# Kernel tuning notes

Measured on AMD Instinct MI355X. Metric: run time of the kernel, lower is better.

The kernel has to match this reference:

```python
import jax, jax.numpy as jnp
import numpy as np

N = 100000
E = 800000
IN_FEATS = 128
H_FEATS = 128
HEADS = 4
OUT = H_FEATS // HEADS  # 32
NEG_SLOPE = 0.2  # DGL GATConv default


def gat_conv(x, src, dst, W, attn_l, attn_r, bias):
    """DGL-style GATConv. x: [N, F_in] -> [N, HEADS, OUT]."""
    h = (x @ W).reshape(N, HEADS, OUT)                      # projected features
    el = jnp.sum(h * attn_l, axis=-1)                       # [N, H]
    er = jnp.sum(h * attn_r, axis=-1)                       # [N, H]
    e = jax.nn.leaky_relu(el[src] + er[dst], NEG_SLOPE)     # [E, H] edge logits
    # edge softmax over incoming edges of each dst node
    m = jax.ops.segment_max(e, dst, num_segments=N)          # [N, H]
    ex = jnp.exp(e - m[dst])                                 # [E, H]
    s = jax.ops.segment_sum(ex, dst, num_segments=N)         # [N, H]
    a = ex / s[dst]                                          # [E, H]
    msg = h[src] * a[:, :, None]                             # [E, H, OUT]
    out = jax.ops.segment_sum(msg, dst, num_segments=N)      # [N, H, OUT]
    return out + bias.reshape(1, HEADS, OUT)


def setup_inputs() -> dict:
    key = jax.random.key(0)
    ks = jax.random.split(key, 12)
    feat = jax.random.normal(ks[0], (N, IN_FEATS), dtype=jnp.float32)
    src = jax.random.randint(ks[1], (E,), 0, N)
    dst = jax.random.randint(ks[2], (E,), 0, N)
    s1 = 1.0 / np.sqrt(IN_FEATS)
    s2 = 1.0 / np.sqrt(H_FEATS)
    return {
        "feat": feat,
        "src": src,
        "dst": dst,
        "W1": jax.random.normal(ks[3], (IN_FEATS, HEADS * OUT), dtype=jnp.float32) * s1,
        "al1": jax.random.normal(ks[4], (HEADS, OUT), dtype=jnp.float32) * s2,
        "ar1": jax.random.normal(ks[5], (HEADS, OUT), dtype=jnp.float32) * s2,
        "b1": jnp.zeros((HEADS * OUT,), dtype=jnp.float32),
        "W2": jax.random.normal(ks[6], (H_FEATS, HEADS * OUT), dtype=jnp.float32) * s2,
        "al2": jax.random.normal(ks[7], (HEADS, OUT), dtype=jnp.float32) * s2,
        "ar2": jax.random.normal(ks[8], (HEADS, OUT), dtype=jnp.float32) * s2,
        "b2": jnp.zeros((HEADS * OUT,), dtype=jnp.float32),
    }


def reference(feat, src, dst, W1, al1, ar1, b1, W2, al2, ar2, b2):
    h = gat_conv(feat, src, dst, W1, al1, ar1, b1).reshape(N, H_FEATS)  # flatten(1)
    h = jax.nn.relu(h)
    h = gat_conv(h, src, dst, W2, al2, ar2, b2).mean(axis=1)            # mean over heads
    return h
```

## Files before the change

kernel.cpp:

```cpp
#include <hip/hip_runtime.h>
#include <math.h>

#define N_NODES 100000
#define N_EDGES 800000
#define NEG_SLOPE 0.2f

typedef __attribute__((ext_vector_type(8))) short short8;
typedef __attribute__((ext_vector_type(4))) float floatx4;

__device__ __forceinline__ float lrelu(float x) { return x > 0.f ? x : NEG_SLOPE * x; }

__device__ __forceinline__ unsigned bf16_rne(float f) {
    unsigned u = __float_as_uint(f);
    return (u + 0x7fffu + ((u >> 16) & 1u)) >> 16;
}
__device__ __forceinline__ unsigned bfpack(float lo, float hi) {
    return bf16_rne(lo) | (bf16_rne(hi) << 16);
}
__device__ __forceinline__ float bflo(unsigned p) { return __uint_as_float(p << 16); }
__device__ __forceinline__ float bfhi(unsigned p) { return __uint_as_float(p & 0xffff0000u); }

__global__ void k_hist(const int* __restrict__ dst, int* __restrict__ deg) {
    int e = blockIdx.x * blockDim.x + threadIdx.x;
    if (e < N_EDGES) atomicAdd(&deg[dst[e]], 1);
}

__global__ __launch_bounds__(256) void k_scan1(const int* __restrict__ deg,
                                               int* __restrict__ rs,
                                               int* __restrict__ bsums) {
    __shared__ int sd[256];
    int tid = threadIdx.x;
    int base = blockIdx.x * 1024 + tid * 4;
    int v0 = (base + 0 < N_NODES) ? deg[base + 0] : 0;
    int v1 = (base + 1 < N_NODES) ? deg[base + 1] : 0;
    int v2 = (base + 2 < N_NODES) ? deg[base + 2] : 0;
    int v3 = (base + 3 < N_NODES) ? deg[base + 3] : 0;
    int t = v0 + v1 + v2 + v3;
    sd[tid] = t;
    __syncthreads();
    int incl = t;
    for (int off = 1; off < 256; off <<= 1) {
        int x = (tid >= off) ? sd[tid - off] : 0;
        __syncthreads();
        incl += x;
        sd[tid] = incl;
        __syncthreads();
    }
    int excl = incl - t;
    if (base + 0 < N_NODES) rs[base + 0] = excl;
    if (base + 1 < N_NODES) rs[base + 1] = excl + v0;
    if (base + 2 < N_NODES) rs[base + 2] = excl + v0 + v1;
    if (base + 3 < N_NODES) rs[base + 3] = excl + v0 + v1 + v2;
    if (tid == 255) bsums[blockIdx.x] = incl;
}

__global__ __launch_bounds__(256) void k_scan2(int* __restrict__ bs, int nb) {
    __shared__ int sd[256];
    int tid = threadIdx.x;
    int t = (tid < nb) ? bs[tid] : 0;
    sd[tid] = t;
    __syncthreads();
    int incl = t;
    for (int off = 1; off < 256; off <<= 1) {
        int x = (tid >= off) ? sd[tid - off] : 0;
        __syncthreads();
        incl += x;
        sd[tid] = incl;
        __syncthreads();
    }
    if (tid < nb) bs[tid] = incl - t;
}

__global__ void k_scan3(int* __restrict__ rs, const int* __restrict__ bs,
                        int* __restrict__ cursor) {
    int idx = blockIdx.x * blockDim.x + threadIdx.x;
    if (idx < N_NODES) {
        int v = rs[idx] + bs[idx >> 10];
        rs[idx] = v;
        cursor[idx] = v;
    }
    if (idx == 0) rs[N_NODES] = N_EDGES;
}

__global__ void k_scatter(const int* __restrict__ src, const int* __restrict__ dst,
                          int* __restrict__ cursor, int* __restrict__ csr_src) {
    int e = blockIdx.x * blockDim.x + threadIdx.x;
    if (e < N_EDGES) {
        int d = dst[e];
        int p = atomicAdd(&cursor[d], 1);
        csr_src[p] = src[e];
    }
}

__global__ __launch_bounds__(256) void k_wprep2(const float* __restrict__ W1,
                                                const float* __restrict__ W2,
                                                unsigned short* __restrict__ wt1,
                                                unsigned short* __restrict__ wt2) {
    int tid = blockIdx.x * 256 + threadIdx.x;
    const float* W = (tid < 16384) ? W1 : W2;
    unsigned short* wt = (tid < 16384) ? wt1 : wt2;
    int t = tid & 16383;
    int n = t >> 7, k = t & 127;
    wt[t] = (unsigned short)bf16_rne(W[k * 128 + n]);
}

__global__ __launch_bounds__(256) void k_gemm(const void* __restrict__ Xv,
                                              const unsigned short* __restrict__ wt,
                                              const float* __restrict__ al,
                                              const float* __restrict__ ar,
                                              unsigned* __restrict__ Hb,
                                              float* __restrict__ EL,
                                              float* __restrict__ ER,
                                              int src_bf16) {
    __shared__ unsigned short wsh[128 * 128];
    int tid = threadIdx.x;
    int w = tid >> 6, lane = tid & 63;
    int q = lane >> 4, nl = lane & 15;
    int base = blockIdx.x * 128;

    const uint4* wt4 = (const uint4*)wt;
    #pragma unroll
    for (int i = 0; i < 8; i++) {
        int idx = tid + i * 256;
        int rn = idx >> 4, c8 = idx & 15;
        int kc = c8 >> 2, qq = c8 & 3;
        int slot = rn * 128 + ((kc ^ ((rn >> 2) & 3)) * 4 + (qq ^ (rn & 3))) * 8;
        *(uint4*)&wsh[slot] = wt4[idx];
    }

    short8 afr[2][4];
    int row0 = base + w * 32 + nl;
    if (!src_bf16) {
        const float4* X4 = (const float4*)Xv;
        #pragma unroll
        for (int rt = 0; rt < 2; rt++) {
            int rr = row0 + rt * 16; if (rr > N_NODES - 1) rr = N_NODES - 1;
            const float4* px = X4 + (size_t)rr * 32 + q * 2;
            #pragma unroll
            for (int kc = 0; kc < 4; kc++) {
                float4 u = px[kc * 8], v = px[kc * 8 + 1];
                short8 f;
                f[0] = (short)bf16_rne(u.x); f[1] = (short)bf16_rne(u.y);
                f[2] = (short)bf16_rne(u.z); f[3] = (short)bf16_rne(u.w);
                f[4] = (short)bf16_rne(v.x); f[5] = (short)bf16_rne(v.y);
                f[6] = (short)bf16_rne(v.z); f[7] = (short)bf16_rne(v.w);
                afr[rt][kc] = f;
            }
        }
    } else {
        const unsigned short* Xb = (const unsigned short*)Xv;
        #pragma unroll
        for (int rt = 0; rt < 2; rt++) {
            int rr = row0 + rt * 16; if (rr > N_NODES - 1) rr = N_NODES - 1;
            #pragma unroll
            for (int kc = 0; kc < 4; kc++)
                afr[rt][kc] = *(const short8*)(Xb + (size_t)rr * 128 + kc * 32 + q * 8);
        }
    }

    floatx4 acc[2][8];
    #pragma unroll
    for (int rt = 0; rt < 2; rt++)
        #pragma unroll
        for (int ct = 0; ct < 8; ct++)
            acc[rt][ct] = (floatx4){0.f, 0.f, 0.f, 0.f};

    __syncthreads();

    int sw_hi = (nl >> 2) & 3, sw_lo = nl & 3;
    #pragma unroll
    for (int ct = 0; ct < 8; ct++) {
        int rbase = (ct * 16 + nl) * 128;
        #pragma unroll
        for (int kc = 0; kc < 4; kc++) {
            short8 b = *(const short8*)&wsh[rbase + ((kc ^ sw_hi) * 4 + (q ^ sw_lo)) * 8];
            acc[0][ct] = __builtin_amdgcn_mfma_f32_16x16x32_bf16(afr[0][kc], b, acc[0][ct], 0, 0, 0);
            acc[1][ct] = __builtin_amdgcn_mfma_f32_16x16x32_bf16(afr[1][kc], b, acc[1][ct], 0, 0, 0);
        }
    }

    float all_[4], alh_[4], arl_[4], arh_[4];
    #pragma unroll
    for (int h = 0; h < 4; h++) {
        all_[h] = al[h * 32 + nl]; alh_[h] = al[h * 32 + 16 + nl];
        arl_[h] = ar[h * 32 + nl]; arh_[h] = ar[h * 32 + 16 + nl];
    }
    #pragma unroll
    for (int rt = 0; rt < 2; rt++) {
        #pragma unroll
        for (int r = 0; r < 4; r++) {
            int row = base + w * 32 + rt * 16 + q * 4 + r;
            bool valid = row < N_NODES;
            unsigned* hrow = Hb + (size_t)row * 64;
            #pragma unroll
            for (int ct = 0; ct < 8; ct++) {
                float vlo = acc[rt][ct][r];
                float vhi = __shfl_down(vlo, 1);
                if (valid && !(nl & 1)) hrow[ct * 8 + (nl >> 1)] = bfpack(vlo, vhi);
            }
            #pragma unroll
            for (int h = 0; h < 4; h++) {
                float pel = acc[rt][2 * h][r] * all_[h] + acc[rt][2 * h + 1][r] * alh_[h];
                float per = acc[rt][2 * h][r] * arl_[h] + acc[rt][2 * h + 1][r] * arh_[h];
                #pragma unroll
                for (int o = 1; o < 16; o <<= 1) {
                    pel += __shfl_xor(pel, o);
                    per += __shfl_xor(per, o);
                }
                if (valid && nl == 0) { EL[row * 4 + h] = pel; ER[row * 4 + h] = per; }
            }
        }
    }
}

__global__ __launch_bounds__(256) void k_gather(const int* __restrict__ rs,
                                                const int* __restrict__ csr_src,
                                                const float* __restrict__ EL,
                                                const float* __restrict__ ER,
                                                const unsigned* __restrict__ Hb,
                                                const float* __restrict__ bias,
                                                void* __restrict__ out,
                                                int final_layer) {
    int wid = (blockIdx.x * blockDim.x + threadIdx.x) >> 6;
    int lane = threadIdx.x & 63;
    int g = lane >> 4, l16 = lane & 15;
    int h = l16 >> 2;
    int n0 = wid * 4;
    if (n0 >= N_NODES) return;
    int nend = min(n0 + 4, N_NODES);

    float bv[8];
    #pragma unroll
    for (int c = 0; c < 8; c++) bv[c] = bias[l16 * 8 + c];

    for (int n = n0; n < nend; n++) {
        int s = rs[n], e = rs[n + 1];
        float erh = ER[n * 4 + h];
        float acc[8];
        #pragma unroll
        for (int c = 0; c < 8; c++) acc[c] = 0.f;
        float sa = 0.f;

        for (int j = s; j < e; j += 8) {
            int j0 = j + g, j1 = j + 4 + g;
            uint4 p0 = make_uint4(0, 0, 0, 0), p1 = make_uint4(0, 0, 0, 0);
            float w0 = 0.f, w1 = 0.f;
            if (j0 < e) {
                int s0 = csr_src[j0];
                p0 = *(const uint4*)(Hb + (size_t)s0 * 64 + l16 * 4);
                w0 = __expf(lrelu(EL[s0 * 4 + h] + erh));
            }
            if (j1 < e) {
                int s1 = csr_src[j1];
                p1 = *(const uint4*)(Hb + (size_t)s1 * 64 + l16 * 4);
                w1 = __expf(lrelu(EL[s1 * 4 + h] + erh));
            }
            sa += w0 + w1;
            acc[0] = fmaf(bflo(p0.x), w0, acc[0]); acc[1] = fmaf(bfhi(p0.x), w0, acc[1]);
            acc[2] = fmaf(bflo(p0.y), w0, acc[2]); acc[3] = fmaf(bfhi(p0.y), w0, acc[3]);
            acc[4] = fmaf(bflo(p0.z), w0, acc[4]); acc[5] = fmaf(bfhi(p0.z), w0, acc[5]);
            acc[6] = fmaf(bflo(p0.w), w0, acc[6]); acc[7] = fmaf(bfhi(p0.w), w0, acc[7]);
            acc[0] = fmaf(bflo(p1.x), w1, acc[0]); acc[1] = fmaf(bfhi(p1.x), w1, acc[1]);
            acc[2] = fmaf(bflo(p1.y), w1, acc[2]); acc[3] = fmaf(bfhi(p1.y), w1, acc[3]);
            acc[4] = fmaf(bflo(p1.z), w1, acc[4]); acc[5] = fmaf(bfhi(p1.z), w1, acc[5]);
            acc[6] = fmaf(bflo(p1.w), w1, acc[6]); acc[7] = fmaf(bfhi(p1.w), w1, acc[7]);
        }

        #pragma unroll
        for (int c = 0; c < 8; c++) {
            acc[c] += __shfl_xor(acc[c], 16);
            acc[c] += __shfl_xor(acc[c], 32);
        }
        sa += __shfl_xor(sa, 16);
        sa += __shfl_xor(sa, 32);
        float inv = (e > s) ? 1.f / sa : 0.f;

        float r[8];
        #pragma unroll
        for (int c = 0; c < 8; c++) r[c] = acc[c] * inv + bv[c];

        if (!final_layer) {
            if (g == 0) {
                uint4 pk;
                pk.x = bfpack(fmaxf(r[0], 0.f), fmaxf(r[1], 0.f));
                pk.y = bfpack(fmaxf(r[2], 0.f), fmaxf(r[3], 0.f));
                pk.z = bfpack(fmaxf(r[4], 0.f), fmaxf(r[5], 0.f));
                pk.w = bfpack(fmaxf(r[6], 0.f), fmaxf(r[7], 0.f));
                *(uint4*)((unsigned*)out + (size_t)n * 64 + l16 * 4) = pk;
            }
        } else {
            #pragma unroll
            for (int c = 0; c < 8; c++) {
                r[c] += __shfl_xor(r[c], 4);
                r[c] += __shfl_xor(r[c], 8);
            }
            if (g == 0 && l16 < 4) {
                float* po = (float*)out + (size_t)n * 32 + l16 * 8;
                *(float4*)po = make_float4(0.25f * r[0], 0.25f * r[1], 0.25f * r[2], 0.25f * r[3]);
                *(float4*)(po + 4) = make_float4(0.25f * r[4], 0.25f * r[5], 0.25f * r[6], 0.25f * r[7]);
            }
        }
    }
}

extern "C" void kernel_launch(void* const* d_in, const int* in_sizes, int n_in,
                              void* d_out, int out_size, void* d_ws, size_t ws_size,
                              hipStream_t stream) {
    const float* feat = (const float*)d_in[0];
    const int* src = (const int*)d_in[1];
    const int* dst = (const int*)d_in[2];
    const float* W1 = (const float*)d_in[3];
    const float* al1 = (const float*)d_in[4];
    const float* ar1 = (const float*)d_in[5];
    const float* b1 = (const float*)d_in[6];
    const float* W2 = (const float*)d_in[7];
    const float* al2 = (const float*)d_in[8];
    const float* ar2 = (const float*)d_in[9];
    const float* b2 = (const float*)d_in[10];
    float* out = (float*)d_out;

    char* ws = (char*)d_ws;
    size_t off = 0;
    auto alloc = [&](size_t bytes) {
        void* p = ws + off;
        off += (bytes + 255) & ~(size_t)255;
        return p;
    };
    int* deg = (int*)alloc((size_t)N_NODES * 4);
    int* rs = (int*)alloc(((size_t)N_NODES + 1) * 4);
    int* cursor = (int*)alloc((size_t)N_NODES * 4);
    int* bsums = (int*)alloc(128 * 4);
    int* csr_src = (int*)alloc((size_t)N_EDGES * 4);
    unsigned* Hb = (unsigned*)alloc((size_t)N_NODES * 64 * 4);
    float* el = (float*)alloc((size_t)N_NODES * 4 * 4);
    float* er = (float*)alloc((size_t)N_NODES * 4 * 4);
    unsigned* out1b = (unsigned*)alloc((size_t)N_NODES * 64 * 4);
    unsigned short* wt1 = (unsigned short*)alloc(128 * 128 * 2);
    unsigned short* wt2 = (unsigned short*)alloc(128 * 128 * 2);

    hipMemsetAsync(deg, 0, (size_t)N_NODES * 4, stream);

    k_hist<<<(N_EDGES + 255) / 256, 256, 0, stream>>>(dst, deg);
    k_scan1<<<98, 256, 0, stream>>>(deg, rs, bsums);
    k_scan2<<<1, 256, 0, stream>>>(bsums, 98);
    k_scan3<<<(N_NODES + 255) / 256, 256, 0, stream>>>(rs, bsums, cursor);
    k_scatter<<<(N_EDGES + 255) / 256, 256, 0, stream>>>(src, dst, cursor, csr_src);
    k_wprep2<<<128, 256, 0, stream>>>(W1, W2, wt1, wt2);

    int gemm_blocks = (N_NODES + 127) / 128;
    int gat_blocks = (N_NODES + 15) / 16;

    k_gemm<<<gemm_blocks, 256, 0, stream>>>(feat, wt1, al1, ar1, Hb, el, er, 0);
    k_gather<<<gat_blocks, 256, 0, stream>>>(rs, csr_src, el, er, Hb, b1, out1b, 0);
    k_gemm<<<gemm_blocks, 256, 0, stream>>>(out1b, wt2, al2, ar2, Hb, el, er, 1);
    k_gather<<<gat_blocks, 256, 0, stream>>>(rs, csr_src, el, er, Hb, b2, out, 1);
}
```

Before: 338.6 us.

## Fuse preprocessing kernels, single-pass decoupled scan, and prefetch next node's first edges in gather

Merges the degree histogram and weight bf16 conversion into one launch. It replaces the three-kernel scan with one kernel that publishes block sums and spin-waits on a global counter, which relies on all 98 blocks being resident at once. In the gather kernel, the first batch of each next node's edges (csr index, feature row, EL) is loaded early to overlap latency with the current node's work. Together these cut launch count and serial latency, at the cost of a grid-wide spin barrier and higher register use.

```diff
diff --git a/kernel.cpp b/kernel.cpp
--- a/kernel.cpp
+++ b/kernel.cpp
@@ -20,17 +20,44 @@
 __device__ __forceinline__ float bflo(unsigned p) { return __uint_as_float(p << 16); }
 __device__ __forceinline__ float bfhi(unsigned p) { return __uint_as_float(p & 0xffff0000u); }
 
-__global__ void k_hist(const int* __restrict__ dst, int* __restrict__ deg) {
-    int e = blockIdx.x * blockDim.x + threadIdx.x;
-    if (e < N_EDGES) atomicAdd(&deg[dst[e]], 1);
-}
-
-__global__ __launch_bounds__(256) void k_scan1(const int* __restrict__ deg,
-                                               int* __restrict__ rs,
-                                               int* __restrict__ bsums) {
+#define ACC8(P, W)                                                   \
+    acc[0] = fmaf(bflo((P).x), (W), acc[0]);                         \
+    acc[1] = fmaf(bfhi((P).x), (W), acc[1]);                         \
+    acc[2] = fmaf(bflo((P).y), (W), acc[2]);                         \
+    acc[3] = fmaf(bfhi((P).y), (W), acc[3]);                         \
+    acc[4] = fmaf(bflo((P).z), (W), acc[4]);                         \
+    acc[5] = fmaf(bfhi((P).z), (W), acc[5]);                         \
+    acc[6] = fmaf(bflo((P).w), (W), acc[6]);                         \
+    acc[7] = fmaf(bfhi((P).w), (W), acc[7]);
+
+__global__ __launch_bounds__(256) void k_hist_wprep(const int* __restrict__ dst,
+                                                    int* __restrict__ deg,
+                                                    const float* __restrict__ W1,
+                                                    const float* __restrict__ W2,
+                                                    unsigned short* __restrict__ wt1,
+                                                    unsigned short* __restrict__ wt2) {
+    int b = blockIdx.x;
+    if (b < 3125) {
+        int e = b * 256 + threadIdx.x;
+        if (e < N_EDGES) atomicAdd(&deg[dst[e]], 1);
+    } else {
+        int tid = (b - 3125) * 256 + threadIdx.x;
+        const float* W = (tid < 16384) ? W1 : W2;
+        unsigned short* wt = (tid < 16384) ? wt1 : wt2;
+        int t = tid & 16383;
+        int n = t >> 7, k = t & 127;
+        wt[t] = (unsigned short)bf16_rne(W[k * 128 + n]);
+    }
+}
+
+__global__ __launch_bounds__(256) void k_scan(const int* __restrict__ deg,
+                                              int* __restrict__ rs,
+                                              int* __restrict__ cursor,
+                                              int* __restrict__ bsums,
+                                              int* __restrict__ done) {
     __shared__ int sd[256];
-    int tid = threadIdx.x;
-    int base = blockIdx.x * 1024 + tid * 4;
+    int tid = threadIdx.x, b = blockIdx.x;
+    int base = b * 1024 + tid * 4;
     int v0 = (base + 0 < N_NODES) ? deg[base + 0] : 0;
     int v1 = (base + 1 < N_NODES) ? deg[base + 1] : 0;
     int v2 = (base + 2 < N_NODES) ? deg[base + 2] : 0;
@@ -47,39 +74,33 @@
         __syncthreads();
     }
     int excl = incl - t;
-    if (base + 0 < N_NODES) rs[base + 0] = excl;
-    if (base + 1 < N_NODES) rs[base + 1] = excl + v0;
-    if (base + 2 < N_NODES) rs[base + 2] = excl + v0 + v1;
-    if (base + 3 < N_NODES) rs[base + 3] = excl + v0 + v1 + v2;
-    if (tid == 255) bsums[blockIdx.x] = incl;
-}
-
-__global__ __launch_bounds__(256) void k_scan2(int* __restrict__ bs, int nb) {
-    __shared__ int sd[256];
-    int tid = threadIdx.x;
-    int t = (tid < nb) ? bs[tid] : 0;
-    sd[tid] = t;
-    __syncthreads();
-    int incl = t;
-    for (int off = 1; off < 256; off <<= 1) {
-        int x = (tid >= off) ? sd[tid - off] : 0;
+
+    if (tid == 255) {
+        atomicExch(&bsums[b], incl);
+        __threadfence();
+        atomicAdd(done, 1);
+    }
+    if (tid == 0) {
+        while (atomicAdd(done, 0) < 98) { }
+    }
+    __syncthreads();
+
+    int bv = (tid < b) ? atomicAdd(&bsums[tid], 0) : 0;
+    __syncthreads();
+    sd[tid] = bv;
+    __syncthreads();
+    for (int off = 128; off > 0; off >>= 1) {
+        if (tid < off) sd[tid] += sd[tid + off];
         __syncthreads();
-        incl += x;
-        sd[tid] = incl;
-        __syncthreads();
-    }
-    if (tid < nb) bs[tid] = incl - t;
-}
-
-__global__ void k_scan3(int* __restrict__ rs, const int* __restrict__ bs,
-                        int* __restrict__ cursor) {
-    int idx = blockIdx.x * blockDim.x + threadIdx.x;
-    if (idx < N_NODES) {
-        int v = rs[idx] + bs[idx >> 10];
-        rs[idx] = v;
-        cursor[idx] = v;
-    }
-    if (idx == 0) rs[N_NODES] = N_EDGES;
+    }
+    int boff = sd[0];
+
+    int p0 = excl + boff;
+    if (base + 0 < N_NODES) { rs[base + 0] = p0; cursor[base + 0] = p0; }
+    if (base + 1 < N_NODES) { rs[base + 1] = p0 + v0; cursor[base + 1] = p0 + v0; }
+    if (base + 2 < N_NODES) { rs[base + 2] = p0 + v0 + v1; cursor[base + 2] = p0 + v0 + v1; }
+    if (base + 3 < N_NODES) { rs[base + 3] = p0 + v0 + v1 + v2; cursor[base + 3] = p0 + v0 + v1 + v2; }
+    if (b == 0 && tid == 0) rs[N_NODES] = N_EDGES;
 }
 
 __global__ void k_scatter(const int* __restrict__ src, const int* __restrict__ dst,
@@ -90,18 +111,6 @@
         int p = atomicAdd(&cursor[d], 1);
         csr_src[p] = src[e];
     }
-}
-
-__global__ __launch_bounds__(256) void k_wprep2(const float* __restrict__ W1,
-                                                const float* __restrict__ W2,
-                                                unsigned short* __restrict__ wt1,
-                                                unsigned short* __restrict__ wt2) {
-    int tid = blockIdx.x * 256 + threadIdx.x;
-    const float* W = (tid < 16384) ? W1 : W2;
-    unsigned short* wt = (tid < 16384) ? wt1 : wt2;
-    int t = tid & 16383;
-    int n = t >> 7, k = t & 127;
-    wt[t] = (unsigned short)bf16_rne(W[k * 128 + n]);
 }
 
 __global__ __launch_bounds__(256) void k_gemm(const void* __restrict__ Xv,
@@ -214,7 +223,7 @@
 }
 
 __global__ __launch_bounds__(256) void k_gather(const int* __restrict__ rs,
-                                                const int* __restrict__ csr_src,
+                                                const int* __restrict__ csr,
                                                 const float* __restrict__ EL,
                                                 const float* __restrict__ ER,
                                                 const unsigned* __restrict__ Hb,
@@ -227,43 +236,73 @@
     int h = l16 >> 2;
     int n0 = wid * 4;
     if (n0 >= N_NODES) return;
-    int nend = min(n0 + 4, N_NODES);
+    int nlast = min(4, N_NODES - n0);
 
     float bv[8];
     #pragma unroll
     for (int c = 0; c < 8; c++) bv[c] = bias[l16 * 8 + c];
 
-    for (int n = n0; n < nend; n++) {
-        int s = rs[n], e = rs[n + 1];
-        float erh = ER[n * 4 + h];
-        float acc[8];
-        #pragma unroll
-        for (int c = 0; c < 8; c++) acc[c] = 0.f;
-        float sa = 0.f;
-
-        for (int j = s; j < e; j += 8) {
+    int sE[5];
+    #pragma unroll
+    for (int i = 0; i < 5; i++) sE[i] = rs[min(n0 + i, N_NODES)];
+    float erh[4];
+    #pragma unroll
+    for (int i = 0; i < 4; i++) erh[i] = (n0 + i < N_NODES) ? ER[(n0 + i) * 4 + h] : 0.f;
+
+    const uint4 zero4 = make_uint4(0, 0, 0, 0);
+
+    int cs0 = 0, cs1 = 0; bool cv0, cv1;
+    {
+        int s = sE[0], e = sE[1];
+        cv0 = (s + g) < e; cv1 = (s + 4 + g) < e;
+        if (cv0) cs0 = csr[s + g];
+        if (cv1) cs1 = csr[s + 4 + g];
+    }
+    uint4 cp0 = zero4, cp1 = zero4;
+    float cel0 = 0.f, cel1 = 0.f;
+    if (cv0) { cp0 = *(const uint4*)(Hb + (size_t)cs0 * 64 + l16 * 4); cel0 = EL[cs0 * 4 + h]; }
+    if (cv1) { cp1 = *(const uint4*)(Hb + (size_t)cs1 * 64 + l16 * 4); cel1 = EL[cs1 * 4 + h]; }
+
+    for (int nn = 0; nn < nlast; nn++) {
+        int s = sE[nn], e = sE[nn + 1];
+
+        int ns0 = 0, ns1 = 0; bool nv0 = false, nv1 = false;
+        if (nn + 1 < nlast) {
+            int s2 = sE[nn + 1], e2 = sE[nn + 2];
+            nv0 = (s2 + g) < e2; nv1 = (s2 + 4 + g) < e2;
+            if (nv0) ns0 = csr[s2 + g];
+            if (nv1) ns1 = csr[s2 + 4 + g];
+        }
+
+        float acc[8] = {0.f, 0.f, 0.f, 0.f, 0.f, 0.f, 0.f, 0.f};
+        float w0 = cv0 ? __expf(lrelu(cel0 + erh[nn])) : 0.f;
+        float w1 = cv1 ? __expf(lrelu(cel1 + erh[nn])) : 0.f;
+        float sa = w0 + w1;
+        ACC8(cp0, w0);
+        ACC8(cp1, w1);
+
+        for (int j = s + 8; j < e; j += 8) {
             int j0 = j + g, j1 = j + 4 + g;
-            uint4 p0 = make_uint4(0, 0, 0, 0), p1 = make_uint4(0, 0, 0, 0);
-            float w0 = 0.f, w1 = 0.f;
-            if (j0 < e) {
-                int s0 = csr_src[j0];
-                p0 = *(const uint4*)(Hb + (size_t)s0 * 64 + l16 * 4);
-                w0 = __expf(lrelu(EL[s0 * 4 + h] + erh));
-            }
-            if (j1 < e) {
-                int s1 = csr_src[j1];
-                p1 = *(const uint4*)(Hb + (size_t)s1 * 64 + l16 * 4);
-                w1 = __expf(lrelu(EL[s1 * 4 + h] + erh));
-            }
-            sa += w0 + w1;
-            acc[0] = fmaf(bflo(p0.x), w0, acc[0]); acc[1] = fmaf(bfhi(p0.x), w0, acc[1]);
-            acc[2] = fmaf(bflo(p0.y), w0, acc[2]); acc[3] = fmaf(bfhi(p0.y), w0, acc[3]);
-            acc[4] = fmaf(bflo(p0.z), w0, acc[4]); acc[5] = fmaf(bfhi(p0.z), w0, acc[5]);
-            acc[6] = fmaf(bflo(p0.w), w0, acc[6]); acc[7] = fmaf(bfhi(p0.w), w0, acc[7]);
-            acc[0] = fmaf(bflo(p1.x), w1, acc[0]); acc[1] = fmaf(bfhi(p1.x), w1, acc[1]);
-            acc[2] = fmaf(bflo(p1.y), w1, acc[2]); acc[3] = fmaf(bfhi(p1.y), w1, acc[3]);
-            acc[4] = fmaf(bflo(p1.z), w1, acc[4]); acc[5] = fmaf(bfhi(p1.z), w1, acc[5]);
-            acc[6] = fmaf(bflo(p1.w), w1, acc[6]); acc[7] = fmaf(bfhi(p1.w), w1, acc[7]);
+            bool b0 = j0 < e, b1 = j1 < e;
+            int t0 = 0, t1 = 0;
+            if (b0) t0 = csr[j0];
+            if (b1) t1 = csr[j1];
+            uint4 p0 = zero4, p1 = zero4;
+            float e0 = 0.f, e1 = 0.f;
+            if (b0) { p0 = *(const uint4*)(Hb + (size_t)t0 * 64 + l16 * 4); e0 = EL[t0 * 4 + h]; }
+            if (b1) { p1 = *(const uint4*)(Hb + (size_t)t1 * 64 + l16 * 4); e1 = EL[t1 * 4 + h]; }
+            float x0 = b0 ? __expf(lrelu(e0 + erh[nn])) : 0.f;
+            float x1 = b1 ? __expf(lrelu(e1 + erh[nn])) : 0.f;
+            sa += x0 + x1;
+            ACC8(p0, x0);
+            ACC8(p1, x1);
+        }
+
+        if (nn + 1 < nlast) {
+            cp0 = zero4; cp1 = zero4; cel0 = 0.f; cel1 = 0.f;
+            if (nv0) { cp0 = *(const uint4*)(Hb + (size_t)ns0 * 64 + l16 * 4); cel0 = EL[ns0 * 4 + h]; }
+            if (nv1) { cp1 = *(const uint4*)(Hb + (size_t)ns1 * 64 + l16 * 4); cel1 = EL[ns1 * 4 + h]; }
+            cv0 = nv0; cv1 = nv1;
         }
 
         #pragma unroll
@@ -275,6 +314,7 @@
         sa += __shfl_xor(sa, 32);
         float inv = (e > s) ? 1.f / sa : 0.f;
 
+        int n = n0 + nn;
         float r[8];
         #pragma unroll
         for (int c = 0; c < 8; c++) r[c] = acc[c] * inv + bv[c];
@@ -327,6 +367,7 @@
         return p;
     };
     int* deg = (int*)alloc((size_t)N_NODES * 4);
+    int* done = (int*)alloc(256);
     int* rs = (int*)alloc(((size_t)N_NODES + 1) * 4);
     int* cursor = (int*)alloc((size_t)N_NODES * 4);
     int* bsums = (int*)alloc(128 * 4);
@@ -338,14 +379,12 @@
     unsigned short* wt1 = (unsigned short*)alloc(128 * 128 * 2);
     unsigned short* wt2 = (unsigned short*)alloc(128 * 128 * 2);
 
-    hipMemsetAsync(deg, 0, (size_t)N_NODES * 4, stream);
-
-    k_hist<<<(N_EDGES + 255) / 256, 256, 0, stream>>>(dst, deg);
-    k_scan1<<<98, 256, 0, stream>>>(deg, rs, bsums);
-    k_scan2<<<1, 256, 0, stream>>>(bsums, 98);
-    k_scan3<<<(N_NODES + 255) / 256, 256, 0, stream>>>(rs, bsums, cursor);
+    size_t zbytes = (size_t)((char*)done - (char*)deg) + 256;
+    hipMemsetAsync(deg, 0, zbytes, stream);
+
+    k_hist_wprep<<<3125 + 128, 256, 0, stream>>>(dst, deg, W1, W2, wt1, wt2);
+    k_scan<<<98, 256, 0, stream>>>(deg, rs, cursor, bsums, done);
     k_scatter<<<(N_EDGES + 255) / 256, 256, 0, stream>>>(src, dst, cursor, csr_src);
-    k_wprep2<<<128, 256, 0, stream>>>(W1, W2, wt1, wt2);
 
     int gemm_blocks = (N_NODES + 127) / 128;
     int gat_blocks = (N_NODES + 15) / 16;
```

After: 362.9 us. 7.2% more time.

## Merge preprocessing kernels and stage GEMM input tiles through shared memory

Applied to the files above, without the earlier changes.

Fuses the degree histogram with weight conversion into one launch, and replaces the three-kernel scan with a single kernel that uses a spin-wait grid barrier on an atomic counter to pick up the block offsets. This cuts kernel launches and the gaps between them. The GEMM now loads its input rows cooperatively with coalesced wide loads into a swizzled shared-memory tile before building MFMA fragments. That doubles shared memory use per block, which may lower occupancy, and the spin barrier assumes all 98 scan blocks are resident at once.

```diff
diff --git a/kernel.cpp b/kernel.cpp
--- a/kernel.cpp
+++ b/kernel.cpp
@@ -20,17 +20,34 @@
 __device__ __forceinline__ float bflo(unsigned p) { return __uint_as_float(p << 16); }
 __device__ __forceinline__ float bfhi(unsigned p) { return __uint_as_float(p & 0xffff0000u); }
 
-__global__ void k_hist(const int* __restrict__ dst, int* __restrict__ deg) {
-    int e = blockIdx.x * blockDim.x + threadIdx.x;
-    if (e < N_EDGES) atomicAdd(&deg[dst[e]], 1);
-}
-
-__global__ __launch_bounds__(256) void k_scan1(const int* __restrict__ deg,
-                                               int* __restrict__ rs,
-                                               int* __restrict__ bsums) {
+__global__ __launch_bounds__(256) void k_hist_wprep(const int* __restrict__ dst,
+                                                    int* __restrict__ deg,
+                                                    const float* __restrict__ W1,
+                                                    const float* __restrict__ W2,
+                                                    unsigned short* __restrict__ wt1,
+                                                    unsigned short* __restrict__ wt2) {
+    int b = blockIdx.x;
+    if (b < 3125) {
+        int e = b * 256 + threadIdx.x;
+        if (e < N_EDGES) atomicAdd(&deg[dst[e]], 1);
+    } else {
+        int tid = (b - 3125) * 256 + threadIdx.x;
+        const float* W = (tid < 16384) ? W1 : W2;
+        unsigned short* wt = (tid < 16384) ? wt1 : wt2;
+        int t = tid & 16383;
+        int n = t >> 7, k = t & 127;
+        wt[t] = (unsigned short)bf16_rne(W[k * 128 + n]);
+    }
+}
+
+__global__ __launch_bounds__(256) void k_scan(const int* __restrict__ deg,
+                                              int* __restrict__ rs,
+                                              int* __restrict__ cursor,
+                                              int* __restrict__ bsums,
+                                              int* __restrict__ done) {
     __shared__ int sd[256];
-    int tid = threadIdx.x;
-    int base = blockIdx.x * 1024 + tid * 4;
+    int tid = threadIdx.x, b = blockIdx.x;
+    int base = b * 1024 + tid * 4;
     int v0 = (base + 0 < N_NODES) ? deg[base + 0] : 0;
     int v1 = (base + 1 < N_NODES) ? deg[base + 1] : 0;
     int v2 = (base + 2 < N_NODES) ? deg[base + 2] : 0;
@@ -47,39 +64,33 @@
         __syncthreads();
     }
     int excl = incl - t;
-    if (base + 0 < N_NODES) rs[base + 0] = excl;
-    if (base + 1 < N_NODES) rs[base + 1] = excl + v0;
-    if (base + 2 < N_NODES) rs[base + 2] = excl + v0 + v1;
-    if (base + 3 < N_NODES) rs[base + 3] = excl + v0 + v1 + v2;
-    if (tid == 255) bsums[blockIdx.x] = incl;
-}
-
-__global__ __launch_bounds__(256) void k_scan2(int* __restrict__ bs, int nb) {
-    __shared__ int sd[256];
-    int tid = threadIdx.x;
-    int t = (tid < nb) ? bs[tid] : 0;
-    sd[tid] = t;
-    __syncthreads();
-    int incl = t;
-    for (int off = 1; off < 256; off <<= 1) {
-        int x = (tid >= off) ? sd[tid - off] : 0;
+
+    if (tid == 255) {
+        atomicExch(&bsums[b], incl);
+        __threadfence();
+        atomicAdd(done, 1);
+    }
+    if (tid == 0) {
+        while (atomicAdd(done, 0) < 98) { }
+    }
+    __syncthreads();
+
+    int bv = (tid < b) ? atomicAdd(&bsums[tid], 0) : 0;
+    __syncthreads();
+    sd[tid] = bv;
+    __syncthreads();
+    for (int off = 128; off > 0; off >>= 1) {
+        if (tid < off) sd[tid] += sd[tid + off];
         __syncthreads();
-        incl += x;
-        sd[tid] = incl;
-        __syncthreads();
-    }
-    if (tid < nb) bs[tid] = incl - t;
-}
-
-__global__ void k_scan3(int* __restrict__ rs, const int* __restrict__ bs,
-                        int* __restrict__ cursor) {
-    int idx = blockIdx.x * blockDim.x + threadIdx.x;
-    if (idx < N_NODES) {
-        int v = rs[idx] + bs[idx >> 10];
-        rs[idx] = v;
-        cursor[idx] = v;
-    }
-    if (idx == 0) rs[N_NODES] = N_EDGES;
+    }
+    int boff = sd[0];
+
+    int p0 = excl + boff;
+    if (base + 0 < N_NODES) { rs[base + 0] = p0; cursor[base + 0] = p0; }
+    if (base + 1 < N_NODES) { rs[base + 1] = p0 + v0; cursor[base + 1] = p0 + v0; }
+    if (base + 2 < N_NODES) { rs[base + 2] = p0 + v0 + v1; cursor[base + 2] = p0 + v0 + v1; }
+    if (base + 3 < N_NODES) { rs[base + 3] = p0 + v0 + v1 + v2; cursor[base + 3] = p0 + v0 + v1 + v2; }
+    if (b == 0 && tid == 0) rs[N_NODES] = N_EDGES;
 }
 
 __global__ void k_scatter(const int* __restrict__ src, const int* __restrict__ dst,
@@ -90,18 +101,6 @@
         int p = atomicAdd(&cursor[d], 1);
         csr_src[p] = src[e];
     }
-}
-
-__global__ __launch_bounds__(256) void k_wprep2(const float* __restrict__ W1,
-                                                const float* __restrict__ W2,
-                                                unsigned short* __restrict__ wt1,
-                                                unsigned short* __restrict__ wt2) {
-    int tid = blockIdx.x * 256 + threadIdx.x;
-    const float* W = (tid < 16384) ? W1 : W2;
-    unsigned short* wt = (tid < 16384) ? wt1 : wt2;
-    int t = tid & 16383;
-    int n = t >> 7, k = t & 127;
-    wt[t] = (unsigned short)bf16_rne(W[k * 128 + n]);
 }
 
 __global__ __launch_bounds__(256) void k_gemm(const void* __restrict__ Xv,
@@ -113,6 +112,7 @@
                                               float* __restrict__ ER,
                                               int src_bf16) {
     __shared__ unsigned short wsh[128 * 128];
+    __shared__ unsigned short xsh[128 * 128];
     int tid = threadIdx.x;
     int w = tid >> 6, lane = tid & 63;
     int q = lane >> 4, nl = lane & 15;
@@ -128,34 +128,46 @@
         *(uint4*)&wsh[slot] = wt4[idx];
     }
 
-    short8 afr[2][4];
-    int row0 = base + w * 32 + nl;
     if (!src_bf16) {
         const float4* X4 = (const float4*)Xv;
         #pragma unroll
-        for (int rt = 0; rt < 2; rt++) {
-            int rr = row0 + rt * 16; if (rr > N_NODES - 1) rr = N_NODES - 1;
-            const float4* px = X4 + (size_t)rr * 32 + q * 2;
-            #pragma unroll
-            for (int kc = 0; kc < 4; kc++) {
-                float4 u = px[kc * 8], v = px[kc * 8 + 1];
-                short8 f;
-                f[0] = (short)bf16_rne(u.x); f[1] = (short)bf16_rne(u.y);
-                f[2] = (short)bf16_rne(u.z); f[3] = (short)bf16_rne(u.w);
-                f[4] = (short)bf16_rne(v.x); f[5] = (short)bf16_rne(v.y);
-                f[6] = (short)bf16_rne(v.z); f[7] = (short)bf16_rne(v.w);
-                afr[rt][kc] = f;
-            }
+        for (int i = 0; i < 8; i++) {
+            int idx = tid + i * 256;
+            int rn = idx >> 4, c8 = idx & 15;
+            int rr = base + rn; if (rr >= N_NODES) rr = N_NODES - 1;
+            float4 a = X4[(size_t)rr * 32 + c8 * 2];
+            float4 bb = X4[(size_t)rr * 32 + c8 * 2 + 1];
+            int kc = c8 >> 2, qq = c8 & 3;
+            int slot = rn * 128 + ((kc ^ ((rn >> 2) & 3)) * 4 + (qq ^ (rn & 3))) * 8;
+            uint4 pk;
+            pk.x = bfpack(a.x, a.y); pk.y = bfpack(a.z, a.w);
+            pk.z = bfpack(bb.x, bb.y); pk.w = bfpack(bb.z, bb.w);
+            *(uint4*)&xsh[slot] = pk;
         }
     } else {
-        const unsigned short* Xb = (const unsigned short*)Xv;
-        #pragma unroll
-        for (int rt = 0; rt < 2; rt++) {
-            int rr = row0 + rt * 16; if (rr > N_NODES - 1) rr = N_NODES - 1;
-            #pragma unroll
-            for (int kc = 0; kc < 4; kc++)
-                afr[rt][kc] = *(const short8*)(Xb + (size_t)rr * 128 + kc * 32 + q * 8);
-        }
+        const uint4* Xb4 = (const uint4*)Xv;
+        #pragma unroll
+        for (int i = 0; i < 8; i++) {
+            int idx = tid + i * 256;
+            int rn = idx >> 4, c8 = idx & 15;
+            int rr = base + rn; if (rr >= N_NODES) rr = N_NODES - 1;
+            int kc = c8 >> 2, qq = c8 & 3;
+            int slot = rn * 128 + ((kc ^ ((rn >> 2) & 3)) * 4 + (qq ^ (rn & 3))) * 8;
+            *(uint4*)&xsh[slot] = Xb4[(size_t)rr * 16 + c8];
+        }
+    }
+
+    __syncthreads();
+
+    int sw_hi = (nl >> 2) & 3, sw_lo = nl & 3;
+
+    short8 afr[2][4];
+    #pragma unroll
+    for (int rt = 0; rt < 2; rt++) {
+        int r = w * 32 + rt * 16 + nl;
+        #pragma unroll
+        for (int kc = 0; kc < 4; kc++)
+            afr[rt][kc] = *(const short8*)&xsh[r * 128 + ((kc ^ sw_hi) * 4 + (q ^ sw_lo)) * 8];
     }
 
     floatx4 acc[2][8];
@@ -165,9 +177,6 @@
         for (int ct = 0; ct < 8; ct++)
             acc[rt][ct] = (floatx4){0.f, 0.f, 0.f, 0.f};
 
-    __syncthreads();
-
-    int sw_hi = (nl >> 2) & 3, sw_lo = nl & 3;
     #pragma unroll
     for (int ct = 0; ct < 8; ct++) {
         int rbase = (ct * 16 + nl) * 128;
@@ -327,6 +336,7 @@
         return p;
     };
     int* deg = (int*)alloc((size_t)N_NODES * 4);
+    int* done = (int*)alloc(256);
     int* rs = (int*)alloc(((size_t)N_NODES + 1) * 4);
     int* cursor = (int*)alloc((size_t)N_NODES * 4);
     int* bsums = (int*)alloc(128 * 4);
@@ -338,14 +348,12 @@
     unsigned short* wt1 = (unsigned short*)alloc(128 * 128 * 2);
     unsigned short* wt2 = (unsigned short*)alloc(128 * 128 * 2);
 
-    hipMemsetAsync(deg, 0, (size_t)N_NODES * 4, stream);
-
-    k_hist<<<(N_EDGES + 255) / 256, 256, 0, stream>>>(dst, deg);
-    k_scan1<<<98, 256, 0, stream>>>(deg, rs, bsums);
-    k_scan2<<<1, 256, 0, stream>>>(bsums, 98);
-    k_scan3<<<(N_NODES + 255) / 256, 256, 0, stream>>>(rs, bsums, cursor);
+    size_t zbytes = (size_t)((char*)done - (char*)deg) + 256;
+    hipMemsetAsync(deg, 0, zbytes, stream);
+
+    k_hist_wprep<<<3125 + 128, 256, 0, stream>>>(dst, deg, W1, W2, wt1, wt2);
+    k_scan<<<98, 256, 0, stream>>>(deg, rs, cursor, bsums, done);
     k_scatter<<<(N_EDGES + 255) / 256, 256, 0, stream>>>(src, dst, cursor, csr_src);
-    k_wprep2<<<128, 256, 0, stream>>>(W1, W2, wt1, wt2);
 
     int gemm_blocks = (N_NODES + 127) / 128;
     int gat_blocks = (N_NODES + 15) / 16;
```

After: 344.8 us. No clear change (+1.8%).
